# Kernel tuning notes

Measured on AMD Instinct MI355X. Metric: run time of the kernel, lower is better.

Reference implementation:

```python
import jax, jax.numpy as jnp
import numpy as np
from jax.scipy.special import logsumexp

COST_GAMMA = 0.1
MIN_ZERO_GAMMA = 0.1
_CLIP = 1.0 - 1e-7


def setup_inputs() -> dict:
    key = jax.random.key(0)
    k1, k2, k3 = jax.random.split(key, 3)
    B, D, K = 65536, 128, 1024
    xs = jax.random.normal(k1, (B, D), dtype=jnp.float32)
    xs = xs / jnp.linalg.norm(xs, axis=-1, keepdims=True)  # points on sphere S^{D-1}
    mus = jax.random.normal(k2, (D, K), dtype=jnp.float32)  # prototype params (pre-projx)
    alphas = jax.random.uniform(k3, (K,), dtype=jnp.float32)
    return {"xs": xs, "mus": mus, "alphas": alphas}


def reference(xs, mus, alphas):
    # projx: project prototype columns onto the unit sphere
    mus_p = mus / jnp.linalg.norm(mus, axis=0, keepdims=True)  # [D, K]
    # sphere cost: half squared geodesic distance, cdist-like [B, K]
    ip = jnp.clip(xs @ mus_p, -_CLIP, _CLIP)
    costs = 0.5 * jnp.arccos(ip) ** 2 + alphas  # [B, K]
    # softmin over components via stable logsumexp
    F = COST_GAMMA * logsumexp(-costs / COST_GAMMA, axis=1)  # [B]
    # soft min(F, 0): logsumexp over stacked (F, 0) == logaddexp
    F = MIN_ZERO_GAMMA * jnp.logaddexp(-F / MIN_ZERO_GAMMA, 0.0)
    return F
```

## Files before the change

kernel.cpp:

```cpp
#include <hip/hip_runtime.h>
#include <hip/hip_bf16.h>


typedef __attribute__((ext_vector_type(8))) short short8;
typedef __attribute__((ext_vector_type(4))) float f32x4;
typedef __attribute__((ext_vector_type(2))) float f32x2;

#define KP 1024
#define DD 128

__device__ __forceinline__ unsigned int f2bf(float f) {
  unsigned int u = __float_as_uint(f);
  return (u + 0x7FFFu + ((u >> 16) & 1u)) >> 16;
}

__device__ __forceinline__ f32x2 pk_fma(f32x2 a, f32x2 b, f32x2 c) {
  return __builtin_elementwise_fma(a, b, c);
}

__global__ __launch_bounds__(256) void prep_kernel(
    const float* __restrict__ mus, const float* __restrict__ alphas,
    uint4* __restrict__ musbf_sw, float* __restrict__ lw) {
  __shared__ float psum[8][32];
  __shared__ float Tt[32][129];
  __shared__ float inv_s[32];
  const int t = threadIdx.x;
  const int k0 = blockIdx.x * 32;
  const int kk = t & 31, gg = t >> 5;
  float s = 0.0f;
  for (int i = 0; i < 16; ++i) {
    float v = mus[(gg * 16 + i) * KP + k0 + kk];
    s = fmaf(v, v, s);
  }
  psum[gg][kk] = s;
  __syncthreads();
  if (t < 32) {
    float tot = 0.0f;
    for (int j = 0; j < 8; ++j) tot += psum[j][t];
    inv_s[t] = rsqrtf(tot);
    lw[k0 + t] = -14.4269504089f * alphas[k0 + t];
  }
  for (int i = 0; i < 16; ++i) {
    int e = i * 256 + t;
    Tt[e & 31][e >> 5] = mus[(e >> 5) * KP + k0 + (e & 31)];
  }
  __syncthreads();
  #pragma unroll
  for (int i = 0; i < 2; ++i) {
    int u = i * 256 + t;
    int w0 = u >> 5, c32 = u & 31;
    int col = k0 + c32;
    float inv = inv_s[c32];
    uint4 o;
    o.x = f2bf(Tt[c32][w0 * 8 + 0] * inv) | (f2bf(Tt[c32][w0 * 8 + 1] * inv) << 16);
    o.y = f2bf(Tt[c32][w0 * 8 + 2] * inv) | (f2bf(Tt[c32][w0 * 8 + 3] * inv) << 16);
    o.z = f2bf(Tt[c32][w0 * 8 + 4] * inv) | (f2bf(Tt[c32][w0 * 8 + 5] * inv) << 16);
    o.w = f2bf(Tt[c32][w0 * 8 + 6] * inv) | (f2bf(Tt[c32][w0 * 8 + 7] * inv) << 16);
    musbf_sw[((col >> 6) << 10) + (w0 << 6) + (col & 63)] = o;
  }
}

__global__ __launch_bounds__(256, 4) void main_kernel(
    const float* __restrict__ xs, const uint4* __restrict__ musbf_sw,
    const float* __restrict__ lw, float* __restrict__ out) {
  __shared__ __align__(16) unsigned short Bs[2][8192];
  const int t = threadIdx.x;
  const int wv = t >> 6, ln = t & 63, q = ln >> 4, l15 = ln & 15;

  const int row = blockIdx.x * 64 + wv * 16 + l15;
  const float4* xs4 = (const float4*)xs;
  const int base4 = row * 32 + q * 2;
  short8 afr[4];
  #pragma unroll
  for (int kkk = 0; kkk < 4; ++kkk) {
    float4 f0 = xs4[base4 + kkk * 8];
    float4 f1 = xs4[base4 + kkk * 8 + 1];
    union { short8 s; uint4 u; } a;
    a.u.x = f2bf(f0.x) | (f2bf(f0.y) << 16);
    a.u.y = f2bf(f0.z) | (f2bf(f0.w) << 16);
    a.u.z = f2bf(f1.x) | (f2bf(f1.y) << 16);
    a.u.w = f2bf(f1.z) | (f2bf(f1.w) << 16);
    afr[kkk] = a.s;
  }

  uint4 v[4];
  #pragma unroll
  for (int i = 0; i < 4; ++i) v[i] = musbf_sw[i * 256 + t];
  #pragma unroll
  for (int i = 0; i < 4; ++i) *(uint4*)&Bs[0][(i * 256 + t) * 8] = v[i];
  __syncthreads();

  const f32x2 C_mh = {-0.5f, -0.5f}, C_ph = {0.5f, 0.5f};
  const f32x2 C_z0 = {0.0f, 0.0f};
  const f32x2 C5 = {-3.6067376f, -3.6067376f};
  const f32x2 C4 = {-2.3449500f, -2.3449500f};
  const f32x2 C3 = {-3.2975886f, -3.2975886f};
  const f32x2 C2 = {-5.1295823f, -5.1295823f};
  const f32x2 C1 = {-9.6179669f, -9.6179669f};
  const f32x2 C0 = {-28.8539008f, -28.8539008f};

  f32x2 sums2[2] = {(f32x2){0.f, 0.f}, (f32x2){0.f, 0.f}};

  for (int cg = 0; cg < 16; ++cg) {
    if (cg < 15) {
      #pragma unroll
      for (int i = 0; i < 4; ++i)
        v[i] = musbf_sw[(cg + 1) * 1024 + i * 256 + t];
    }
    float lwv[4];
    #pragma unroll
    for (int nt = 0; nt < 4; ++nt) lwv[nt] = lw[cg * 64 + nt * 16 + l15];

    f32x4 acc[4];
    #pragma unroll
    for (int nt = 0; nt < 4; ++nt) acc[nt] = (f32x4){0.f, 0.f, 0.f, 0.f};
    const unsigned short* bp = &Bs[cg & 1][q * 512 + l15 * 8];
    #pragma unroll
    for (int kkk = 0; kkk < 4; ++kkk)
      #pragma unroll
      for (int nt = 0; nt < 4; ++nt) {
        short8 b = *(const short8*)(bp + kkk * 2048 + nt * 128);
        acc[nt] = __builtin_amdgcn_mfma_f32_16x16x32_bf16(afr[kkk], b, acc[nt], 0, 0, 0);
      }

    #pragma unroll
    for (int nt = 0; nt < 4; ++nt) {
      f32x2 lwp = {lwv[nt], lwv[nt]};
      #pragma unroll
      for (int p = 0; p < 2; ++p) {
        f32x2 x = {acc[nt][2 * p], acc[nt][2 * p + 1]};
        f32x2 z = pk_fma(x, C_mh, C_ph);
        z = __builtin_elementwise_max(z, C_z0);
        f32x2 h = pk_fma(z, C5, C4);
        h = pk_fma(z, h, C3);
        h = pk_fma(z, h, C2);
        h = pk_fma(z, h, C1);
        h = pk_fma(z, h, C0);
        f32x2 arg = pk_fma(z, h, lwp);
        f32x2 e = {__builtin_amdgcn_exp2f(arg.x), __builtin_amdgcn_exp2f(arg.y)};
        sums2[p] = sums2[p] + e;
      }
    }

    if (cg < 15) {
      #pragma unroll
      for (int i = 0; i < 4; ++i)
        *(uint4*)&Bs[(cg + 1) & 1][(i * 256 + t) * 8] = v[i];
      __syncthreads();
    }
  }

  float s[4] = {sums2[0].x, sums2[0].y, sums2[1].x, sums2[1].y};
  #pragma unroll
  for (int s2 = 1; s2 < 16; s2 <<= 1)
    #pragma unroll
    for (int r = 0; r < 4; ++r) s[r] += __shfl_xor(s[r], s2, 64);
  if (l15 == 0) {
    #pragma unroll
    for (int r = 0; r < 4; ++r)
      out[blockIdx.x * 64 + wv * 16 + q * 4 + r] = 0.1f * log1pf(1.0f / s[r]);
  }
}

extern "C" void kernel_launch(void* const* d_in, const int* in_sizes, int n_in,
                              void* d_out, int out_size, void* d_ws, size_t ws_size,
                              hipStream_t stream) {
  const float* xs     = (const float*)d_in[0];
  const float* mus    = (const float*)d_in[1];
  const float* alphas = (const float*)d_in[2];
  float* out = (float*)d_out;

  uint4* musbf_sw = (uint4*)d_ws;
  float* lw = (float*)((char*)d_ws + 16384 * sizeof(uint4));

  prep_kernel<<<KP / 32, 256, 0, stream>>>(mus, alphas, musbf_sw, lw);
  const int B = in_sizes[0] / DD;
  main_kernel<<<B / 64, 256, 0, stream>>>(xs, musbf_sw, lw, out);
}
```

Baseline: 107.9 us.

## Give each wave two 16-row tiles so LDS B-fragments are reused

Each block now uses 2 waves instead of 4, and each wave processes 32 rows (two 16-row MFMA tiles) that share every B fragment read from LDS. Each ds_read therefore feeds two MFMAs, which halves LDS read traffic per output row. The cost is more registers per thread (double accumulators and A fragments), fewer waves per block, and the lower launch-bounds occupancy hint of 2, which may hurt latency hiding for the exp/polynomial phase.

```diff
diff --git a/kernel.cpp b/kernel.cpp
--- a/kernel.cpp
+++ b/kernel.cpp
@@ -60,34 +60,37 @@
   }
 }
 
-__global__ __launch_bounds__(256, 4) void main_kernel(
+__global__ __launch_bounds__(128, 2) void main_kernel(
     const float* __restrict__ xs, const uint4* __restrict__ musbf_sw,
     const float* __restrict__ lw, float* __restrict__ out) {
   __shared__ __align__(16) unsigned short Bs[2][8192];
   const int t = threadIdx.x;
   const int wv = t >> 6, ln = t & 63, q = ln >> 4, l15 = ln & 15;
 
-  const int row = blockIdx.x * 64 + wv * 16 + l15;
+  const int row0 = blockIdx.x * 64 + wv * 32 + l15;
   const float4* xs4 = (const float4*)xs;
-  const int base4 = row * 32 + q * 2;
-  short8 afr[4];
+  short8 afr[2][4];
   #pragma unroll
-  for (int kkk = 0; kkk < 4; ++kkk) {
-    float4 f0 = xs4[base4 + kkk * 8];
-    float4 f1 = xs4[base4 + kkk * 8 + 1];
-    union { short8 s; uint4 u; } a;
-    a.u.x = f2bf(f0.x) | (f2bf(f0.y) << 16);
-    a.u.y = f2bf(f0.z) | (f2bf(f0.w) << 16);
-    a.u.z = f2bf(f1.x) | (f2bf(f1.y) << 16);
-    a.u.w = f2bf(f1.z) | (f2bf(f1.w) << 16);
-    afr[kkk] = a.s;
+  for (int rt = 0; rt < 2; ++rt) {
+    const int base4 = (row0 + rt * 16) * 32 + q * 2;
+    #pragma unroll
+    for (int kkk = 0; kkk < 4; ++kkk) {
+      float4 f0 = xs4[base4 + kkk * 8];
+      float4 f1 = xs4[base4 + kkk * 8 + 1];
+      union { short8 s; uint4 u; } a;
+      a.u.x = f2bf(f0.x) | (f2bf(f0.y) << 16);
+      a.u.y = f2bf(f0.z) | (f2bf(f0.w) << 16);
+      a.u.z = f2bf(f1.x) | (f2bf(f1.y) << 16);
+      a.u.w = f2bf(f1.z) | (f2bf(f1.w) << 16);
+      afr[rt][kkk] = a.s;
+    }
   }
 
-  uint4 v[4];
+  uint4 v[8];
   #pragma unroll
-  for (int i = 0; i < 4; ++i) v[i] = musbf_sw[i * 256 + t];
+  for (int i = 0; i < 8; ++i) v[i] = musbf_sw[i * 128 + t];
   #pragma unroll
-  for (int i = 0; i < 4; ++i) *(uint4*)&Bs[0][(i * 256 + t) * 8] = v[i];
+  for (int i = 0; i < 8; ++i) *(uint4*)&Bs[0][(i * 128 + t) * 8] = v[i];
   __syncthreads();
 
   const f32x2 C_mh = {-0.5f, -0.5f}, C_ph = {0.5f, 0.5f};
@@ -99,66 +102,77 @@
   const f32x2 C1 = {-9.6179669f, -9.6179669f};
   const f32x2 C0 = {-28.8539008f, -28.8539008f};
 
-  f32x2 sums2[2] = {(f32x2){0.f, 0.f}, (f32x2){0.f, 0.f}};
+  f32x2 sums2[2][2] = {{(f32x2){0.f, 0.f}, (f32x2){0.f, 0.f}},
+                       {(f32x2){0.f, 0.f}, (f32x2){0.f, 0.f}}};
 
   for (int cg = 0; cg < 16; ++cg) {
     if (cg < 15) {
       #pragma unroll
-      for (int i = 0; i < 4; ++i)
-        v[i] = musbf_sw[(cg + 1) * 1024 + i * 256 + t];
+      for (int i = 0; i < 8; ++i)
+        v[i] = musbf_sw[(cg + 1) * 1024 + i * 128 + t];
     }
     float lwv[4];
     #pragma unroll
     for (int nt = 0; nt < 4; ++nt) lwv[nt] = lw[cg * 64 + nt * 16 + l15];
 
-    f32x4 acc[4];
+    f32x4 acc[2][4];
     #pragma unroll
-    for (int nt = 0; nt < 4; ++nt) acc[nt] = (f32x4){0.f, 0.f, 0.f, 0.f};
+    for (int rt = 0; rt < 2; ++rt)
+      #pragma unroll
+      for (int nt = 0; nt < 4; ++nt) acc[rt][nt] = (f32x4){0.f, 0.f, 0.f, 0.f};
+
     const unsigned short* bp = &Bs[cg & 1][q * 512 + l15 * 8];
     #pragma unroll
     for (int kkk = 0; kkk < 4; ++kkk)
       #pragma unroll
       for (int nt = 0; nt < 4; ++nt) {
         short8 b = *(const short8*)(bp + kkk * 2048 + nt * 128);
-        acc[nt] = __builtin_amdgcn_mfma_f32_16x16x32_bf16(afr[kkk], b, acc[nt], 0, 0, 0);
+        acc[0][nt] = __builtin_amdgcn_mfma_f32_16x16x32_bf16(afr[0][kkk], b, acc[0][nt], 0, 0, 0);
+        acc[1][nt] = __builtin_amdgcn_mfma_f32_16x16x32_bf16(afr[1][kkk], b, acc[1][nt], 0, 0, 0);
       }
 
     #pragma unroll
-    for (int nt = 0; nt < 4; ++nt) {
-      f32x2 lwp = {lwv[nt], lwv[nt]};
+    for (int rt = 0; rt < 2; ++rt)
       #pragma unroll
-      for (int p = 0; p < 2; ++p) {
-        f32x2 x = {acc[nt][2 * p], acc[nt][2 * p + 1]};
-        f32x2 z = pk_fma(x, C_mh, C_ph);
-        z = __builtin_elementwise_max(z, C_z0);
-        f32x2 h = pk_fma(z, C5, C4);
-        h = pk_fma(z, h, C3);
-        h = pk_fma(z, h, C2);
-        h = pk_fma(z, h, C1);
-        h = pk_fma(z, h, C0);
-        f32x2 arg = pk_fma(z, h, lwp);
-        f32x2 e = {__builtin_amdgcn_exp2f(arg.x), __builtin_amdgcn_exp2f(arg.y)};
-        sums2[p] = sums2[p] + e;
+      for (int nt = 0; nt < 4; ++nt) {
+        f32x2 lwp = {lwv[nt], lwv[nt]};
+        #pragma unroll
+        for (int p = 0; p < 2; ++p) {
+          f32x2 x = {acc[rt][nt][2 * p], acc[rt][nt][2 * p + 1]};
+          f32x2 z = pk_fma(x, C_mh, C_ph);
+          z = __builtin_elementwise_max(z, C_z0);
+          f32x2 h = pk_fma(z, C5, C4);
+          h = pk_fma(z, h, C3);
+          h = pk_fma(z, h, C2);
+          h = pk_fma(z, h, C1);
+          h = pk_fma(z, h, C0);
+          f32x2 arg = pk_fma(z, h, lwp);
+          f32x2 e = {__builtin_amdgcn_exp2f(arg.x), __builtin_amdgcn_exp2f(arg.y)};
+          sums2[rt][p] = sums2[rt][p] + e;
+        }
       }
-    }
 
     if (cg < 15) {
       #pragma unroll
-      for (int i = 0; i < 4; ++i)
-        *(uint4*)&Bs[(cg + 1) & 1][(i * 256 + t) * 8] = v[i];
+      for (int i = 0; i < 8; ++i)
+        *(uint4*)&Bs[(cg + 1) & 1][(i * 128 + t) * 8] = v[i];
       __syncthreads();
     }
   }
 
-  float s[4] = {sums2[0].x, sums2[0].y, sums2[1].x, sums2[1].y};
   #pragma unroll
-  for (int s2 = 1; s2 < 16; s2 <<= 1)
+  for (int rt = 0; rt < 2; ++rt) {
+    float s[4] = {sums2[rt][0].x, sums2[rt][0].y, sums2[rt][1].x, sums2[rt][1].y};
     #pragma unroll
-    for (int r = 0; r < 4; ++r) s[r] += __shfl_xor(s[r], s2, 64);
-  if (l15 == 0) {
-    #pragma unroll
-    for (int r = 0; r < 4; ++r)
-      out[blockIdx.x * 64 + wv * 16 + q * 4 + r] = 0.1f * log1pf(1.0f / s[r]);
+    for (int s2 = 1; s2 < 16; s2 <<= 1)
+      #pragma unroll
+      for (int r = 0; r < 4; ++r) s[r] += __shfl_xor(s[r], s2, 64);
+    if (l15 == 0) {
+      #pragma unroll
+      for (int r = 0; r < 4; ++r)
+        out[blockIdx.x * 64 + wv * 32 + rt * 16 + q * 4 + r] =
+            0.1f * log1pf(1.0f / s[r]);
+    }
   }
 }
 
@@ -175,5 +189,5 @@
 
   prep_kernel<<<KP / 32, 256, 0, stream>>>(mus, alphas, musbf_sw, lw);
   const int B = in_sizes[0] / DD;
-  main_kernel<<<B / 64, 256, 0, stream>>>(xs, musbf_sw, lw, out);
+  main_kernel<<<B / 64, 128, 0, stream>>>(xs, musbf_sw, lw, out);
 }
```

Measured after the change: 108.4 us. About the same (+0.5%).

## Read prototype fragments directly from global memory and split K across two waves

Applied to the files above, without the earlier changes.

Drops the LDS double-buffered staging of the bf16 prototype matrix and its per-chunk barriers. Each wave now loads its B fragments straight from global/L2. Blocks shrink to 128 threads covering 16 rows, with the two waves each handling half of the 1024 components and combining partial sums through a small shared array. This removes the LDS traffic and synchronisation, but each 16-row tile now rereads the whole 256KB B matrix from cache, and the number of blocks grows fourfold.

```diff
diff --git a/kernel.cpp b/kernel.cpp
--- a/kernel.cpp
+++ b/kernel.cpp
@@ -60,14 +60,14 @@
   }
 }
 
-__global__ __launch_bounds__(256, 4) void main_kernel(
+__global__ __launch_bounds__(128, 6) void main_kernel(
     const float* __restrict__ xs, const uint4* __restrict__ musbf_sw,
     const float* __restrict__ lw, float* __restrict__ out) {
-  __shared__ __align__(16) unsigned short Bs[2][8192];
+  __shared__ float part[2][16];
   const int t = threadIdx.x;
   const int wv = t >> 6, ln = t & 63, q = ln >> 4, l15 = ln & 15;
 
-  const int row = blockIdx.x * 64 + wv * 16 + l15;
+  const int row = blockIdx.x * 16 + l15;
   const float4* xs4 = (const float4*)xs;
   const int base4 = row * 32 + q * 2;
   short8 afr[4];
@@ -83,13 +83,6 @@
     afr[kkk] = a.s;
   }
 
-  uint4 v[4];
-  #pragma unroll
-  for (int i = 0; i < 4; ++i) v[i] = musbf_sw[i * 256 + t];
-  #pragma unroll
-  for (int i = 0; i < 4; ++i) *(uint4*)&Bs[0][(i * 256 + t) * 8] = v[i];
-  __syncthreads();
-
   const f32x2 C_mh = {-0.5f, -0.5f}, C_ph = {0.5f, 0.5f};
   const f32x2 C_z0 = {0.0f, 0.0f};
   const f32x2 C5 = {-3.6067376f, -3.6067376f};
@@ -101,12 +94,11 @@
 
   f32x2 sums2[2] = {(f32x2){0.f, 0.f}, (f32x2){0.f, 0.f}};
 
-  for (int cg = 0; cg < 16; ++cg) {
-    if (cg < 15) {
-      #pragma unroll
-      for (int i = 0; i < 4; ++i)
-        v[i] = musbf_sw[(cg + 1) * 1024 + i * 256 + t];
-    }
+  const short8* __restrict__ B8 = (const short8*)musbf_sw;
+  const int ub = q * 64 + l15;
+
+  for (int cgi = 0; cgi < 8; ++cgi) {
+    const int cg = wv * 8 + cgi;
     float lwv[4];
     #pragma unroll
     for (int nt = 0; nt < 4; ++nt) lwv[nt] = lw[cg * 64 + nt * 16 + l15];
@@ -114,14 +106,18 @@
     f32x4 acc[4];
     #pragma unroll
     for (int nt = 0; nt < 4; ++nt) acc[nt] = (f32x4){0.f, 0.f, 0.f, 0.f};
-    const unsigned short* bp = &Bs[cg & 1][q * 512 + l15 * 8];
+
     #pragma unroll
-    for (int kkk = 0; kkk < 4; ++kkk)
-      #pragma unroll
-      for (int nt = 0; nt < 4; ++nt) {
-        short8 b = *(const short8*)(bp + kkk * 2048 + nt * 128);
-        acc[nt] = __builtin_amdgcn_mfma_f32_16x16x32_bf16(afr[kkk], b, acc[nt], 0, 0, 0);
-      }
+    for (int kkk = 0; kkk < 4; ++kkk) {
+      short8 b0 = B8[cg * 1024 + kkk * 256 + ub];
+      short8 b1 = B8[cg * 1024 + kkk * 256 + ub + 16];
+      short8 b2 = B8[cg * 1024 + kkk * 256 + ub + 32];
+      short8 b3 = B8[cg * 1024 + kkk * 256 + ub + 48];
+      acc[0] = __builtin_amdgcn_mfma_f32_16x16x32_bf16(afr[kkk], b0, acc[0], 0, 0, 0);
+      acc[1] = __builtin_amdgcn_mfma_f32_16x16x32_bf16(afr[kkk], b1, acc[1], 0, 0, 0);
+      acc[2] = __builtin_amdgcn_mfma_f32_16x16x32_bf16(afr[kkk], b2, acc[2], 0, 0, 0);
+      acc[3] = __builtin_amdgcn_mfma_f32_16x16x32_bf16(afr[kkk], b3, acc[3], 0, 0, 0);
+    }
 
     #pragma unroll
     for (int nt = 0; nt < 4; ++nt) {
@@ -141,13 +137,6 @@
         sums2[p] = sums2[p] + e;
       }
     }
-
-    if (cg < 15) {
-      #pragma unroll
-      for (int i = 0; i < 4; ++i)
-        *(uint4*)&Bs[(cg + 1) & 1][(i * 256 + t) * 8] = v[i];
-      __syncthreads();
-    }
   }
 
   float s[4] = {sums2[0].x, sums2[0].y, sums2[1].x, sums2[1].y};
@@ -155,10 +144,15 @@
   for (int s2 = 1; s2 < 16; s2 <<= 1)
     #pragma unroll
     for (int r = 0; r < 4; ++r) s[r] += __shfl_xor(s[r], s2, 64);
+
   if (l15 == 0) {
     #pragma unroll
-    for (int r = 0; r < 4; ++r)
-      out[blockIdx.x * 64 + wv * 16 + q * 4 + r] = 0.1f * log1pf(1.0f / s[r]);
+    for (int r = 0; r < 4; ++r) part[wv][q * 4 + r] = s[r];
+  }
+  __syncthreads();
+  if (t < 16) {
+    float S = part[0][t] + part[1][t];
+    out[blockIdx.x * 16 + t] = 0.1f * log1pf(1.0f / S);
   }
 }
 
@@ -175,5 +169,5 @@
 
   prep_kernel<<<KP / 32, 256, 0, stream>>>(mus, alphas, musbf_sw, lw);
   const int B = in_sizes[0] / DD;
-  main_kernel<<<B / 64, 256, 0, stream>>>(xs, musbf_sw, lw, out);
+  main_kernel<<<B / 16, 128, 0, stream>>>(xs, musbf_sw, lw, out);
 }
```

New measurement: 114.0 us. 1.06x slower.

## Keep prototype tile in registers and stream xs rows, reduce via atomics

Applied to the files above, without the earlier changes.

Restructures the main kernel so each wave holds one 64-column slice of the bf16 prototypes in registers for the whole kernel and loops over 16 row tiles of xs. This removes LDS staging and barriers. Partial exp-sums from the 16 column groups are combined with atomicAdd into a zeroed output, and a separate finalize kernel applies log1p. The cost is that xs is now read by 16 different waves (4 blocks) instead of once, and the change adds a memset, global atomics and an extra launch, with lower occupancy (launch bound 3).

```diff
diff --git a/kernel.cpp b/kernel.cpp
--- a/kernel.cpp
+++ b/kernel.cpp
@@ -60,35 +60,24 @@
   }
 }
 
-__global__ __launch_bounds__(256, 4) void main_kernel(
+__global__ __launch_bounds__(256, 3) void main_kernel(
     const float* __restrict__ xs, const uint4* __restrict__ musbf_sw,
     const float* __restrict__ lw, float* __restrict__ out) {
-  __shared__ __align__(16) unsigned short Bs[2][8192];
   const int t = threadIdx.x;
   const int wv = t >> 6, ln = t & 63, q = ln >> 4, l15 = ln & 15;
+  const int rr = blockIdx.x >> 2;
+  const int g = (blockIdx.x & 3) * 4 + wv;
+  const int row_base = rr * 256;
 
-  const int row = blockIdx.x * 64 + wv * 16 + l15;
-  const float4* xs4 = (const float4*)xs;
-  const int base4 = row * 32 + q * 2;
-  short8 afr[4];
+  const short8* __restrict__ B8 = (const short8*)musbf_sw;
+  short8 bfr[16];
   #pragma unroll
-  for (int kkk = 0; kkk < 4; ++kkk) {
-    float4 f0 = xs4[base4 + kkk * 8];
-    float4 f1 = xs4[base4 + kkk * 8 + 1];
-    union { short8 s; uint4 u; } a;
-    a.u.x = f2bf(f0.x) | (f2bf(f0.y) << 16);
-    a.u.y = f2bf(f0.z) | (f2bf(f0.w) << 16);
-    a.u.z = f2bf(f1.x) | (f2bf(f1.y) << 16);
-    a.u.w = f2bf(f1.z) | (f2bf(f1.w) << 16);
-    afr[kkk] = a.s;
-  }
+  for (int j = 0; j < 16; ++j)
+    bfr[j] = B8[g * 1024 + (j >> 2) * 256 + (j & 3) * 16 + q * 64 + l15];
 
-  uint4 v[4];
+  float lwv[4];
   #pragma unroll
-  for (int i = 0; i < 4; ++i) v[i] = musbf_sw[i * 256 + t];
-  #pragma unroll
-  for (int i = 0; i < 4; ++i) *(uint4*)&Bs[0][(i * 256 + t) * 8] = v[i];
-  __syncthreads();
+  for (int nt = 0; nt < 4; ++nt) lwv[nt] = lw[g * 64 + nt * 16 + l15];
 
   const f32x2 C_mh = {-0.5f, -0.5f}, C_ph = {0.5f, 0.5f};
   const f32x2 C_z0 = {0.0f, 0.0f};
@@ -99,30 +88,34 @@
   const f32x2 C1 = {-9.6179669f, -9.6179669f};
   const f32x2 C0 = {-28.8539008f, -28.8539008f};
 
-  f32x2 sums2[2] = {(f32x2){0.f, 0.f}, (f32x2){0.f, 0.f}};
+  const float4* xs4 = (const float4*)xs;
 
-  for (int cg = 0; cg < 16; ++cg) {
-    if (cg < 15) {
-      #pragma unroll
-      for (int i = 0; i < 4; ++i)
-        v[i] = musbf_sw[(cg + 1) * 1024 + i * 256 + t];
+  for (int rt = 0; rt < 16; ++rt) {
+    const int base4 = (row_base + rt * 16 + l15) * 32 + q * 2;
+    short8 afr[4];
+    #pragma unroll
+    for (int kkk = 0; kkk < 4; ++kkk) {
+      float4 f0 = xs4[base4 + kkk * 8];
+      float4 f1 = xs4[base4 + kkk * 8 + 1];
+      union { short8 s; uint4 u; } a;
+      a.u.x = f2bf(f0.x) | (f2bf(f0.y) << 16);
+      a.u.y = f2bf(f0.z) | (f2bf(f0.w) << 16);
+      a.u.z = f2bf(f1.x) | (f2bf(f1.y) << 16);
+      a.u.w = f2bf(f1.z) | (f2bf(f1.w) << 16);
+      afr[kkk] = a.s;
     }
-    float lwv[4];
-    #pragma unroll
-    for (int nt = 0; nt < 4; ++nt) lwv[nt] = lw[cg * 64 + nt * 16 + l15];
 
     f32x4 acc[4];
     #pragma unroll
     for (int nt = 0; nt < 4; ++nt) acc[nt] = (f32x4){0.f, 0.f, 0.f, 0.f};
-    const unsigned short* bp = &Bs[cg & 1][q * 512 + l15 * 8];
     #pragma unroll
     for (int kkk = 0; kkk < 4; ++kkk)
       #pragma unroll
-      for (int nt = 0; nt < 4; ++nt) {
-        short8 b = *(const short8*)(bp + kkk * 2048 + nt * 128);
-        acc[nt] = __builtin_amdgcn_mfma_f32_16x16x32_bf16(afr[kkk], b, acc[nt], 0, 0, 0);
-      }
+      for (int nt = 0; nt < 4; ++nt)
+        acc[nt] = __builtin_amdgcn_mfma_f32_16x16x32_bf16(
+            afr[kkk], bfr[kkk * 4 + nt], acc[nt], 0, 0, 0);
 
+    f32x2 sums2[2] = {(f32x2){0.f, 0.f}, (f32x2){0.f, 0.f}};
     #pragma unroll
     for (int nt = 0; nt < 4; ++nt) {
       f32x2 lwp = {lwv[nt], lwv[nt]};
@@ -142,24 +135,23 @@
       }
     }
 
-    if (cg < 15) {
+    float s[4] = {sums2[0].x, sums2[0].y, sums2[1].x, sums2[1].y};
+    #pragma unroll
+    for (int s2 = 1; s2 < 16; s2 <<= 1)
       #pragma unroll
-      for (int i = 0; i < 4; ++i)
-        *(uint4*)&Bs[(cg + 1) & 1][(i * 256 + t) * 8] = v[i];
-      __syncthreads();
+      for (int r = 0; r < 4; ++r) s[r] += __shfl_xor(s[r], s2, 64);
+    if (l15 == 0) {
+      #pragma unroll
+      for (int r = 0; r < 4; ++r)
+        atomicAdd(&out[row_base + rt * 16 + q * 4 + r], s[r]);
     }
   }
+}
 
-  float s[4] = {sums2[0].x, sums2[0].y, sums2[1].x, sums2[1].y};
-  #pragma unroll
-  for (int s2 = 1; s2 < 16; s2 <<= 1)
-    #pragma unroll
-    for (int r = 0; r < 4; ++r) s[r] += __shfl_xor(s[r], s2, 64);
-  if (l15 == 0) {
-    #pragma unroll
-    for (int r = 0; r < 4; ++r)
-      out[blockIdx.x * 64 + wv * 16 + q * 4 + r] = 0.1f * log1pf(1.0f / s[r]);
-  }
+__global__ __launch_bounds__(256) void fin_kernel(float* __restrict__ out) {
+  const int i = blockIdx.x * 256 + threadIdx.x;
+  float S = out[i];
+  out[i] = 0.1f * log1pf(1.0f / S);
 }
 
 extern "C" void kernel_launch(void* const* d_in, const int* in_sizes, int n_in,
@@ -173,7 +165,10 @@
   uint4* musbf_sw = (uint4*)d_ws;
   float* lw = (float*)((char*)d_ws + 16384 * sizeof(uint4));
 
+  hipMemsetAsync(out, 0, (size_t)out_size * sizeof(float), stream);
+
   prep_kernel<<<KP / 32, 256, 0, stream>>>(mus, alphas, musbf_sw, lw);
   const int B = in_sizes[0] / DD;
   main_kernel<<<B / 64, 256, 0, stream>>>(xs, musbf_sw, lw, out);
+  fin_kernel<<<B / 256, 256, 0, stream>>>(out);
 }
```

Result: slower. 139.3 us (+29.1%).
